# Kernel tuning notes

Hardware: AMD Instinct MI355X
Metric: run time of the kernel (lower is better)

Reference implementation:

```python
import jax, jax.numpy as jnp
import numpy as np

TOKEN_DIM = 256
NUM_HEADS = 2
IN_DIMS = 512
D = TOKEN_DIM * NUM_HEADS  # 512
SCALE = TOKEN_DIM ** (-0.5)


def _l2norm(v, axis):
    # torch F.normalize: v / max(||v||_2, eps)
    n = jnp.sqrt(jnp.sum(v * v, axis=axis, keepdims=True))
    return v / jnp.maximum(n, 1e-12)


def setup_inputs() -> dict:
    key = jax.random.key(0)
    ks = jax.random.split(key, 10)
    b, n = 8, 4096
    x = jax.random.normal(ks[0], (b, n, IN_DIMS), dtype=jnp.float32)
    s = 0.02
    Wq = jax.random.normal(ks[1], (IN_DIMS, D), dtype=jnp.float32) * s
    bq = jax.random.normal(ks[2], (D,), dtype=jnp.float32) * s
    Wk = jax.random.normal(ks[3], (IN_DIMS, D), dtype=jnp.float32) * s
    bk = jax.random.normal(ks[4], (D,), dtype=jnp.float32) * s
    Wr = jax.random.normal(ks[5], (D, TOKEN_DIM), dtype=jnp.float32) * s
    br = jax.random.normal(ks[6], (TOKEN_DIM,), dtype=jnp.float32) * s
    w_alpha = jax.random.normal(ks[7], (D, 1), dtype=jnp.float32)
    w_beta = jax.random.normal(ks[8], (D, 1), dtype=jnp.float32)
    return {"x": x, "Wq": Wq, "bq": bq, "Wk": Wk, "bk": bk,
            "Wr": Wr, "br": br, "w_alpha": w_alpha, "w_beta": w_beta}


def reference(x, Wq, bq, Wk, bk, Wr, br, w_alpha, w_beta):
    # x: [b, n, in_dims]
    q = x @ Wq + bq                      # [b, n, D]
    k = x @ Wk + bk                      # [b, n, D]
    q = _l2norm(q, axis=-1)
    k = _l2norm(k, axis=-1)
    v = _l2norm(k, axis=-1)              # original bug: value = normalize(key)

    alpha_w = (q @ w_alpha) * SCALE      # [b, n, 1]
    alpha_w = _l2norm(alpha_w, axis=1)   # normalize over token axis
    g_q = jnp.sum(alpha_w * q, axis=1)   # [b, D]
    g_q = jax.nn.softmax(g_q, axis=-1)

    p = g_q[:, None, :] * k              # [b, n, D]
    beta_w = _l2norm((p @ w_beta) * SCALE, axis=1)  # [b, n, 1]
    g_k = jnp.sum(beta_w * p, axis=1)    # [b, D]
    g_k = jax.nn.softmax(g_k, axis=-1)

    kvi = g_k[:, None, :] * v + q        # [b, n, D]
    return kvi @ Wr + br                 # [b, n, token_dim]
```

## Files before the change

kernel.cpp:

```cpp
#include <hip/hip_runtime.h>
#include <hip/hip_bf16.h>
#include <stdint.h>

#define BATCH    8
#define NTOKB    4096
#define NTOK     (BATCH * NTOKB)
#define DIN      512
#define DD       512
#define TD       256
#define SCALE    0.0625f
#define LSTR     36

typedef unsigned short ushortT;
typedef __attribute__((ext_vector_type(8))) short  short8;
typedef __attribute__((ext_vector_type(4))) float  f32x4;

union Frag { uint4 u; short8 s; };

__device__ __forceinline__ float bf_lo(uint32_t u) { return __uint_as_float(u << 16); }
__device__ __forceinline__ float bf_hi(uint32_t u) { return __uint_as_float(u & 0xffff0000u); }
__device__ __forceinline__ float bf2f(ushortT u) { return __uint_as_float(((uint32_t)u) << 16); }
__device__ __forceinline__ ushortT f2bf(float f) {
    uint32_t u = __float_as_uint(f);
    return (ushortT)((u + 0x7fffu + ((u >> 16) & 1u)) >> 16);
}
__device__ __forceinline__ short8 lds_frag(const ushortT* p) {
    uint2 a = *reinterpret_cast<const uint2*>(p);
    uint2 b = *reinterpret_cast<const uint2*>(p + 4);
    Frag f; f.u.x = a.x; f.u.y = a.y; f.u.z = b.x; f.u.w = b.y;
    return f.s;
}

__global__ __launch_bounds__(256) void packw_kernel(
    const float* __restrict__ Wq, const float* __restrict__ Wk,
    const float* __restrict__ Wr, ushortT* __restrict__ W16)
{
    const int blk = blockIdx.x;
    if (blk < 32) {
        const int mat = blk >> 4, c = blk & 15;
        const float* S = mat ? Wk : Wq;
        ushortT* D = W16 + (size_t)mat * (512 * 512) + (size_t)c * 16384;
        for (int i = threadIdx.x; i < 16384; i += 256) {
            int n = i & 511, kk = i >> 9;
            D[n * 32 + kk] = f2bf(S[(size_t)(c * 32 + kk) * 512 + n]);
        }
    } else {
        const int c = blk - 32;
        ushortT* D = W16 + (size_t)2 * (512 * 512) + (size_t)c * 8192;
        for (int i = threadIdx.x; i < 8192; i += 256) {
            int n = i & 255, kk = i >> 8;
            D[n * 32 + kk] = f2bf(Wr[(size_t)(c * 32 + kk) * 256 + n]);
        }
    }
}

__global__ __launch_bounds__(512) void gemm_qk_kernel(
    const float* __restrict__ x, const ushortT* __restrict__ W16,
    const float* __restrict__ bq, const float* __restrict__ bk,
    const float* __restrict__ w_alpha,
    ushortT* __restrict__ qn, ushortT* __restrict__ kn,
    float* __restrict__ alpha_raw)
{
    __shared__ ushortT xs[64 * LSTR];
    __shared__ ushortT wsd[512 * LSTR];
    __shared__ float rowsq[8][64];
    __shared__ float alphap[8][64];
    __shared__ float rnorm_s[64];

    const int tid = threadIdx.x;
    const int mat = blockIdx.y;
    const size_t tok0 = (size_t)blockIdx.x * 64;
    const ushortT* Wb = W16 + (size_t)mat * (512 * 512);
    const float* bias = mat ? bk : bq;
    ushortT* dst = mat ? kn : qn;

    const int lane = tid & 63, w = tid >> 6;
    const int m = lane & 15, quad = lane >> 4;

    f32x4 acc[4][4];
    #pragma unroll
    for (int tr = 0; tr < 4; ++tr)
        #pragma unroll
        for (int tc = 0; tc < 4; ++tc) acc[tr][tc] = (f32x4){0.f, 0.f, 0.f, 0.f};

    const int xtok = tid >> 3;
    const int xkg  = (tid & 7) * 4;
    const float* xsrc = x + (tok0 + xtok) * DIN;
    const int wr_r = tid >> 2;
    const int wseg = (tid & 3) * 8;

    for (int c = 0; c < 16; ++c) {
        __syncthreads();
        {
            float4 xv = *reinterpret_cast<const float4*>(xsrc + c * 32 + xkg);
            ushort4 xb;
            xb.x = f2bf(xv.x); xb.y = f2bf(xv.y); xb.z = f2bf(xv.z); xb.w = f2bf(xv.w);
            *reinterpret_cast<ushort4*>(&xs[xtok * LSTR + xkg]) = xb;
        }
        #pragma unroll
        for (int rr = 0; rr < 4; ++rr) {
            int r = wr_r + rr * 128;
            uint4 gv = *reinterpret_cast<const uint4*>(Wb + (size_t)c * 16384 + r * 32 + wseg);
            uint2* lp = reinterpret_cast<uint2*>(&wsd[r * LSTR + wseg]);
            lp[0] = make_uint2(gv.x, gv.y);
            lp[1] = make_uint2(gv.z, gv.w);
        }
        __syncthreads();
        {
            short8 af[4], bf[4];
            #pragma unroll
            for (int tr = 0; tr < 4; ++tr)
                af[tr] = lds_frag(&xs[(tr * 16 + m) * LSTR + quad * 8]);
            #pragma unroll
            for (int tc = 0; tc < 4; ++tc)
                bf[tc] = lds_frag(&wsd[(w * 64 + tc * 16 + m) * LSTR + quad * 8]);
            #pragma unroll
            for (int tr = 0; tr < 4; ++tr)
                #pragma unroll
                for (int tc = 0; tc < 4; ++tc)
                    acc[tr][tc] = __builtin_amdgcn_mfma_f32_16x16x32_bf16(af[tr], bf[tc], acc[tr][tc], 0, 0, 0);
        }
    }

    float biasv[4], wa[4];
    #pragma unroll
    for (int tc = 0; tc < 4; ++tc) {
        biasv[tc] = bias[w * 64 + tc * 16 + m];
        wa[tc] = (mat == 0) ? w_alpha[w * 64 + tc * 16 + m] : 0.f;
    }
    #pragma unroll
    for (int tr = 0; tr < 4; ++tr)
        #pragma unroll
        for (int tc = 0; tc < 4; ++tc)
            #pragma unroll
            for (int reg = 0; reg < 4; ++reg)
                acc[tr][tc][reg] += biasv[tc];

    __syncthreads();
    #pragma unroll
    for (int tr = 0; tr < 4; ++tr) {
        #pragma unroll
        for (int reg = 0; reg < 4; ++reg) {
            float s = 0.f, a = 0.f;
            #pragma unroll
            for (int tc = 0; tc < 4; ++tc) {
                float v = acc[tr][tc][reg];
                s = fmaf(v, v, s);
                a = fmaf(v, wa[tc], a);
            }
            #pragma unroll
            for (int off = 1; off < 16; off <<= 1) {
                s += __shfl_xor(s, off);
                a += __shfl_xor(a, off);
            }
            if (m == 0) {
                rowsq[w][tr * 16 + quad * 4 + reg] = s;
                alphap[w][tr * 16 + quad * 4 + reg] = a;
            }
        }
    }
    __syncthreads();
    if (tid < 64) {
        float ss = 0.f, aa = 0.f;
        #pragma unroll
        for (int w2 = 0; w2 < 8; ++w2) { ss += rowsq[w2][tid]; aa += alphap[w2][tid]; }
        float rn = 1.0f / fmaxf(sqrtf(ss), 1e-12f);
        rnorm_s[tid] = rn;
        if (mat == 0) alpha_raw[tok0 + tid] = SCALE * aa * rn;
    }
    __syncthreads();
    #pragma unroll
    for (int tr = 0; tr < 4; ++tr) {
        #pragma unroll
        for (int reg = 0; reg < 4; ++reg) {
            float rn = rnorm_s[tr * 16 + quad * 4 + reg];
            size_t row = tok0 + tr * 16 + quad * 4 + reg;
            ushortT* rp = dst + row * DD + w * 64 + m;
            #pragma unroll
            for (int tc = 0; tc < 4; ++tc)
                rp[tc * 16] = f2bf(acc[tr][tc][reg] * rn);
        }
    }
}

__global__ __launch_bounds__(256) void norm_kernel(const float* __restrict__ in,
                                                   float* __restrict__ inv_out)
{
    int b = blockIdx.x;
    __shared__ float red[256];
    float s = 0.f;
    for (int i = threadIdx.x; i < NTOKB; i += 256) {
        float v = in[b * NTOKB + i];
        s = fmaf(v, v, s);
    }
    red[threadIdx.x] = s;
    __syncthreads();
    for (int off = 128; off > 0; off >>= 1) {
        if (threadIdx.x < off) red[threadIdx.x] += red[threadIdx.x + off];
        __syncthreads();
    }
    if (threadIdx.x == 0) inv_out[b] = 1.0f / fmaxf(sqrtf(red[0]), 1e-12f);
}

__global__ __launch_bounds__(256) void wsum_kernel(const ushortT* __restrict__ M,
                                                   const float* __restrict__ raw,
                                                   const float* __restrict__ invp,
                                                   float* __restrict__ dst)
{
    const int blk = blockIdx.x, tid = threadIdx.x;
    const int b = blk >> 5;
    const int i0 = (blk & 31) * 128;
    __shared__ float wr[128];
    if (tid < 128) wr[tid] = raw[(size_t)b * NTOKB + i0 + tid];
    __syncthreads();
    const uint32_t* M32 = reinterpret_cast<const uint32_t*>(M);
    size_t base = ((size_t)b * NTOKB + i0) * 256 + tid;
    float a0 = 0.f, a1 = 0.f;
    for (int ii = 0; ii < 128; ++ii) {
        uint32_t v = M32[base + (size_t)ii * 256];
        float wv = wr[ii];
        a0 = fmaf(wv, bf_lo(v), a0);
        a1 = fmaf(wv, bf_hi(v), a1);
    }
    float iv = invp[b];
    atomicAdd(&dst[b * DD + 2 * tid],     a0 * iv);
    atomicAdd(&dst[b * DD + 2 * tid + 1], a1 * iv);
}

__global__ __launch_bounds__(256) void softmax_kernel(const float* __restrict__ in,
                                                      const float* __restrict__ mul,
                                                      const float* __restrict__ wbeta,
                                                      float* __restrict__ out,
                                                      float* __restrict__ wb2)
{
    int b = blockIdx.x, tid = threadIdx.x;
    __shared__ float red[256];
    float v0 = in[b * DD + tid], v1 = in[b * DD + 256 + tid];
    if (mul) { v0 *= mul[b * DD + tid]; v1 *= mul[b * DD + 256 + tid]; }
    red[tid] = fmaxf(v0, v1);
    __syncthreads();
    for (int off = 128; off > 0; off >>= 1) {
        if (tid < off) red[tid] = fmaxf(red[tid], red[tid + off]);
        __syncthreads();
    }
    float m = red[0];
    __syncthreads();
    float e0 = expf(v0 - m), e1 = expf(v1 - m);
    red[tid] = e0 + e1;
    __syncthreads();
    for (int off = 128; off > 0; off >>= 1) {
        if (tid < off) red[tid] += red[tid + off];
        __syncthreads();
    }
    float rs = 1.0f / red[0];
    float o0 = e0 * rs, o1 = e1 * rs;
    out[b * DD + tid] = o0;
    out[b * DD + 256 + tid] = o1;
    if (wb2) {
        wb2[b * DD + tid]       = o0 * wbeta[tid];
        wb2[b * DD + 256 + tid] = o1 * wbeta[256 + tid];
    }
}

__global__ __launch_bounds__(256) void beta_kernel(const ushortT* __restrict__ kn,
                                                   const float* __restrict__ wb2,
                                                   float* __restrict__ beta_raw)
{
    int wave = threadIdx.x >> 6, lane = threadIdx.x & 63;
    size_t tok = (size_t)blockIdx.x * 4 + wave;
    int b = (int)(tok >> 12);
    uint4 kv = *reinterpret_cast<const uint4*>(kn + tok * DD + lane * 8);
    float4 wv0 = *reinterpret_cast<const float4*>(wb2 + b * DD + lane * 8);
    float4 wv1 = *reinterpret_cast<const float4*>(wb2 + b * DD + lane * 8 + 4);
    float s = bf_lo(kv.x) * wv0.x + bf_hi(kv.x) * wv0.y
            + bf_lo(kv.y) * wv0.z + bf_hi(kv.y) * wv0.w
            + bf_lo(kv.z) * wv1.x + bf_hi(kv.z) * wv1.y
            + bf_lo(kv.w) * wv1.z + bf_hi(kv.w) * wv1.w;
    #pragma unroll
    for (int off = 32; off > 0; off >>= 1) s += __shfl_xor(s, off);
    if (lane == 0) beta_raw[tok] = SCALE * s;
}

__global__ __launch_bounds__(256) void out_mfma_kernel(
    const ushortT* __restrict__ qn, const ushortT* __restrict__ kn,
    const float* __restrict__ g_k, const ushortT* __restrict__ WrT,
    const float* __restrict__ br, float* __restrict__ out)
{
    __shared__ ushortT kvs[64 * LSTR];
    __shared__ ushortT wrs[256 * LSTR];
    __shared__ float gks[512];

    const int tid = threadIdx.x;
    const size_t tok0 = (size_t)blockIdx.x * 64;
    const int b = (int)(tok0 >> 12);

    gks[tid] = g_k[b * DD + tid];
    gks[256 + tid] = g_k[b * DD + 256 + tid];

    const int lane = tid & 63, w = tid >> 6;
    const int m = lane & 15, quad = lane >> 4;

    f32x4 acc[4][4];
    #pragma unroll
    for (int tr = 0; tr < 4; ++tr)
        #pragma unroll
        for (int tc = 0; tc < 4; ++tc) acc[tr][tc] = (f32x4){0.f, 0.f, 0.f, 0.f};

    const int st  = tid >> 2;
    const int skg = (tid & 3) * 8;
    const int wr_r = tid >> 2;
    const int wseg = (tid & 3) * 8;

    for (int c = 0; c < 16; ++c) {
        __syncthreads();
        {
            const size_t base = (tok0 + st) * DD + c * 32 + skg;
            uint4 qv = *reinterpret_cast<const uint4*>(qn + base);
            uint4 kv = *reinterpret_cast<const uint4*>(kn + base);
            const float* g = &gks[c * 32 + skg];
            ushortT o[8];
            o[0] = f2bf(fmaf(g[0], bf_lo(kv.x), bf_lo(qv.x)));
            o[1] = f2bf(fmaf(g[1], bf_hi(kv.x), bf_hi(qv.x)));
            o[2] = f2bf(fmaf(g[2], bf_lo(kv.y), bf_lo(qv.y)));
            o[3] = f2bf(fmaf(g[3], bf_hi(kv.y), bf_hi(qv.y)));
            o[4] = f2bf(fmaf(g[4], bf_lo(kv.z), bf_lo(qv.z)));
            o[5] = f2bf(fmaf(g[5], bf_hi(kv.z), bf_hi(qv.z)));
            o[6] = f2bf(fmaf(g[6], bf_lo(kv.w), bf_lo(qv.w)));
            o[7] = f2bf(fmaf(g[7], bf_hi(kv.w), bf_hi(qv.w)));
            uint2* lp = reinterpret_cast<uint2*>(&kvs[st * LSTR + skg]);
            lp[0] = make_uint2(((uint32_t)o[1] << 16) | o[0], ((uint32_t)o[3] << 16) | o[2]);
            lp[1] = make_uint2(((uint32_t)o[5] << 16) | o[4], ((uint32_t)o[7] << 16) | o[6]);
        }
        #pragma unroll
        for (int rr = 0; rr < 4; ++rr) {
            int r = wr_r + rr * 64;
            uint4 gv = *reinterpret_cast<const uint4*>(WrT + (size_t)c * 8192 + r * 32 + wseg);
            uint2* lp = reinterpret_cast<uint2*>(&wrs[r * LSTR + wseg]);
            lp[0] = make_uint2(gv.x, gv.y);
            lp[1] = make_uint2(gv.z, gv.w);
        }
        __syncthreads();
        {
            short8 af[4], bfr[4];
            #pragma unroll
            for (int tr = 0; tr < 4; ++tr)
                af[tr] = lds_frag(&kvs[(tr * 16 + m) * LSTR + quad * 8]);
            #pragma unroll
            for (int tc = 0; tc < 4; ++tc)
                bfr[tc] = lds_frag(&wrs[(w * 64 + tc * 16 + m) * LSTR + quad * 8]);
            #pragma unroll
            for (int tr = 0; tr < 4; ++tr)
                #pragma unroll
                for (int tc = 0; tc < 4; ++tc)
                    acc[tr][tc] = __builtin_amdgcn_mfma_f32_16x16x32_bf16(af[tr], bfr[tc], acc[tr][tc], 0, 0, 0);
        }
    }

    float brv[4];
    #pragma unroll
    for (int tc = 0; tc < 4; ++tc) brv[tc] = br[w * 64 + tc * 16 + m];
    #pragma unroll
    for (int tr = 0; tr < 4; ++tr) {
        #pragma unroll
        for (int reg = 0; reg < 4; ++reg) {
            size_t row = tok0 + tr * 16 + quad * 4 + reg;
            float* rp = out + row * TD + w * 64 + m;
            #pragma unroll
            for (int tc = 0; tc < 4; ++tc)
                rp[tc * 16] = acc[tr][tc][reg] + brv[tc];
        }
    }
}

extern "C" void kernel_launch(void* const* d_in, const int* in_sizes, int n_in,
                              void* d_out, int out_size, void* d_ws, size_t ws_size,
                              hipStream_t stream)
{
    const float* x       = (const float*)d_in[0];
    const float* Wq      = (const float*)d_in[1];
    const float* bq      = (const float*)d_in[2];
    const float* Wk      = (const float*)d_in[3];
    const float* bk      = (const float*)d_in[4];
    const float* Wr      = (const float*)d_in[5];
    const float* br      = (const float*)d_in[6];
    const float* w_alpha = (const float*)d_in[7];
    const float* w_beta  = (const float*)d_in[8];
    float* out = (float*)d_out;

    ushortT* kn = (ushortT*)d_out;

    char* ws = (char*)d_ws;
    ushortT* qn = (ushortT*)ws;        ws += (size_t)NTOK * DD * sizeof(ushortT);
    ushortT* W16 = (ushortT*)ws;       ws += (size_t)2 * 512 * 512 * sizeof(ushortT)
                                           + (size_t)512 * 256 * sizeof(ushortT);
    float* alpha_raw = (float*)ws;     ws += (size_t)NTOK * sizeof(float);
    float* beta_raw  = (float*)ws;     ws += (size_t)NTOK * sizeof(float);
    float* gq_raw = (float*)ws;        ws += (size_t)BATCH * DD * sizeof(float);
    float* h_raw  = (float*)ws;        ws += (size_t)BATCH * DD * sizeof(float);
    float* g_q    = (float*)ws;        ws += (size_t)BATCH * DD * sizeof(float);
    float* wb2    = (float*)ws;        ws += (size_t)BATCH * DD * sizeof(float);
    float* g_k    = (float*)ws;        ws += (size_t)BATCH * DD * sizeof(float);
    float* inv_a  = (float*)ws;        ws += 64;
    float* inv_b  = (float*)ws;        ws += 64;
    ushortT* WrT = W16 + (size_t)2 * 512 * 512;

    hipMemsetAsync(gq_raw, 0, 2 * BATCH * DD * sizeof(float), stream);

    packw_kernel<<<48, 256, 0, stream>>>(Wq, Wk, Wr, W16);
    gemm_qk_kernel<<<dim3(NTOK / 64, 2), 512, 0, stream>>>(x, W16, bq, bk, w_alpha, qn, kn, alpha_raw);
    norm_kernel<<<BATCH, 256, 0, stream>>>(alpha_raw, inv_a);
    wsum_kernel<<<256, 256, 0, stream>>>(qn, alpha_raw, inv_a, gq_raw);
    softmax_kernel<<<BATCH, 256, 0, stream>>>(gq_raw, nullptr, w_beta, g_q, wb2);
    beta_kernel<<<NTOK / 4, 256, 0, stream>>>(kn, wb2, beta_raw);
    norm_kernel<<<BATCH, 256, 0, stream>>>(beta_raw, inv_b);
    wsum_kernel<<<256, 256, 0, stream>>>(kn, beta_raw, inv_b, h_raw);
    softmax_kernel<<<BATCH, 256, 0, stream>>>(h_raw, g_q, nullptr, g_k, nullptr);
    out_mfma_kernel<<<NTOK / 64, 256, 0, stream>>>(qn, kn, g_k, WrT, br, out);
}
```

Before: 254.4 us.

## Load weight tiles directly into LDS with an XOR-swizzled layout

Weight tiles in both MFMA GEMM kernels are now copied with global_load_lds 16-byte direct-to-LDS loads, so they no longer pass through registers with separate LDS stores. The padded LDS stride is dropped. To avoid bank conflicts without padding, the packing kernel writes the weights pre-swizzled (XOR of the k-group with row bits), and the fragment reads undo the swizzle using single 16-byte LDS loads. This relies on the swizzle matching exactly between the pack and read sides, and on the direct-to-LDS builtin's per-wave addressing layout.

```diff
diff --git a/kernel.cpp b/kernel.cpp
--- a/kernel.cpp
+++ b/kernel.cpp
@@ -30,6 +30,12 @@
     Frag f; f.u.x = a.x; f.u.y = a.y; f.u.z = b.x; f.u.w = b.y;
     return f.s;
 }
+__device__ __forceinline__ void gload_lds16(const ushortT* g, ushortT* l) {
+    __builtin_amdgcn_global_load_lds(
+        (const __attribute__((address_space(1))) uint32_t*)(const void*)g,
+        (__attribute__((address_space(3))) uint32_t*)(void*)l,
+        16, 0, 0);
+}
 
 __global__ __launch_bounds__(256) void packw_kernel(
     const float* __restrict__ Wq, const float* __restrict__ Wk,
@@ -41,15 +47,17 @@
         const float* S = mat ? Wk : Wq;
         ushortT* D = W16 + (size_t)mat * (512 * 512) + (size_t)c * 16384;
         for (int i = threadIdx.x; i < 16384; i += 256) {
-            int n = i & 511, kk = i >> 9;
-            D[n * 32 + kk] = f2bf(S[(size_t)(c * 32 + kk) * 512 + n]);
+            int n = i & 511, p = i >> 9;
+            int l = ((p >> 3) ^ ((n >> 1) & 3)) * 8 + (p & 7);
+            D[n * 32 + p] = f2bf(S[(size_t)(c * 32 + l) * 512 + n]);
         }
     } else {
         const int c = blk - 32;
         ushortT* D = W16 + (size_t)2 * (512 * 512) + (size_t)c * 8192;
         for (int i = threadIdx.x; i < 8192; i += 256) {
-            int n = i & 255, kk = i >> 8;
-            D[n * 32 + kk] = f2bf(Wr[(size_t)(c * 32 + kk) * 256 + n]);
+            int n = i & 255, p = i >> 8;
+            int l = ((p >> 3) ^ ((n >> 1) & 3)) * 8 + (p & 7);
+            D[n * 32 + p] = f2bf(Wr[(size_t)(c * 32 + l) * 256 + n]);
         }
     }
 }
@@ -61,8 +69,8 @@
     ushortT* __restrict__ qn, ushortT* __restrict__ kn,
     float* __restrict__ alpha_raw)
 {
-    __shared__ ushortT xs[64 * LSTR];
-    __shared__ ushortT wsd[512 * LSTR];
+    __shared__ __align__(16) ushortT xs[64 * LSTR];
+    __shared__ __align__(16) ushortT wsd[512 * 32];
     __shared__ float rowsq[8][64];
     __shared__ float alphap[8][64];
     __shared__ float rnorm_s[64];
@@ -86,8 +94,6 @@
     const int xtok = tid >> 3;
     const int xkg  = (tid & 7) * 4;
     const float* xsrc = x + (tok0 + xtok) * DIN;
-    const int wr_r = tid >> 2;
-    const int wseg = (tid & 3) * 8;
 
     for (int c = 0; c < 16; ++c) {
         __syncthreads();
@@ -97,13 +103,13 @@
             xb.x = f2bf(xv.x); xb.y = f2bf(xv.y); xb.z = f2bf(xv.z); xb.w = f2bf(xv.w);
             *reinterpret_cast<ushort4*>(&xs[xtok * LSTR + xkg]) = xb;
         }
-        #pragma unroll
-        for (int rr = 0; rr < 4; ++rr) {
-            int r = wr_r + rr * 128;
-            uint4 gv = *reinterpret_cast<const uint4*>(Wb + (size_t)c * 16384 + r * 32 + wseg);
-            uint2* lp = reinterpret_cast<uint2*>(&wsd[r * LSTR + wseg]);
-            lp[0] = make_uint2(gv.x, gv.y);
-            lp[1] = make_uint2(gv.z, gv.w);
+        {
+            const ushortT* wsrc = Wb + (size_t)c * 16384;
+            #pragma unroll
+            for (int i = 0; i < 4; ++i) {
+                const int region = i * 8 + w;
+                gload_lds16(wsrc + region * 512 + lane * 8, &wsd[region * 512]);
+            }
         }
         __syncthreads();
         {
@@ -112,8 +118,11 @@
             for (int tr = 0; tr < 4; ++tr)
                 af[tr] = lds_frag(&xs[(tr * 16 + m) * LSTR + quad * 8]);
             #pragma unroll
-            for (int tc = 0; tc < 4; ++tc)
-                bf[tc] = lds_frag(&wsd[(w * 64 + tc * 16 + m) * LSTR + quad * 8]);
+            for (int tc = 0; tc < 4; ++tc) {
+                const int n = w * 64 + tc * 16 + m;
+                bf[tc] = *reinterpret_cast<const short8*>(
+                    &wsd[n * 32 + ((quad ^ ((n >> 1) & 3)) * 8)]);
+            }
             #pragma unroll
             for (int tr = 0; tr < 4; ++tr)
                 #pragma unroll
@@ -286,8 +295,8 @@
     const float* __restrict__ g_k, const ushortT* __restrict__ WrT,
     const float* __restrict__ br, float* __restrict__ out)
 {
-    __shared__ ushortT kvs[64 * LSTR];
-    __shared__ ushortT wrs[256 * LSTR];
+    __shared__ __align__(16) ushortT kvs[64 * LSTR];
+    __shared__ __align__(16) ushortT wrs[256 * 32];
     __shared__ float gks[512];
 
     const int tid = threadIdx.x;
@@ -308,8 +317,6 @@
 
     const int st  = tid >> 2;
     const int skg = (tid & 3) * 8;
-    const int wr_r = tid >> 2;
-    const int wseg = (tid & 3) * 8;
 
     for (int c = 0; c < 16; ++c) {
         __syncthreads();
@@ -331,13 +338,13 @@
             lp[0] = make_uint2(((uint32_t)o[1] << 16) | o[0], ((uint32_t)o[3] << 16) | o[2]);
             lp[1] = make_uint2(((uint32_t)o[5] << 16) | o[4], ((uint32_t)o[7] << 16) | o[6]);
         }
-        #pragma unroll
-        for (int rr = 0; rr < 4; ++rr) {
-            int r = wr_r + rr * 64;
-            uint4 gv = *reinterpret_cast<const uint4*>(WrT + (size_t)c * 8192 + r * 32 + wseg);
-            uint2* lp = reinterpret_cast<uint2*>(&wrs[r * LSTR + wseg]);
-            lp[0] = make_uint2(gv.x, gv.y);
-            lp[1] = make_uint2(gv.z, gv.w);
+        {
+            const ushortT* wsrc = WrT + (size_t)c * 8192;
+            #pragma unroll
+            for (int i = 0; i < 4; ++i) {
+                const int region = i * 4 + w;
+                gload_lds16(wsrc + region * 512 + lane * 8, &wrs[region * 512]);
+            }
         }
         __syncthreads();
         {
@@ -346,8 +353,11 @@
             for (int tr = 0; tr < 4; ++tr)
                 af[tr] = lds_frag(&kvs[(tr * 16 + m) * LSTR + quad * 8]);
             #pragma unroll
-            for (int tc = 0; tc < 4; ++tc)
-                bfr[tc] = lds_frag(&wrs[(w * 64 + tc * 16 + m) * LSTR + quad * 8]);
+            for (int tc = 0; tc < 4; ++tc) {
+                const int n = w * 64 + tc * 16 + m;
+                bfr[tc] = *reinterpret_cast<const short8*>(
+                    &wrs[n * 32 + ((quad ^ ((n >> 1) & 3)) * 8)]);
+            }
             #pragma unroll
             for (int tr = 0; tr < 4; ++tr)
                 #pragma unroll
```

Result: faster. 247.7 us (-2.6%).

## Stage full A tile in LDS once and stream weight fragments from global into registers

Applied to the files above, without the earlier changes.

Both MFMA GEMM kernels now load the whole 64xK activation tile into LDS up front with a padded stride, instead of staging per 32-wide K chunk. Weight B fragments are read straight from global memory into registers, double-buffered across K steps, so the weight LDS staging and the two per-chunk barriers go away. The aim is to cut synchronisation and LDS traffic and to overlap weight loads with MFMA work. In exchange, LDS use per block goes up (about 66KB), which may limit occupancy, and the weight reads now depend on L2/global latency being hidden.

```diff
diff --git a/kernel.cpp b/kernel.cpp
--- a/kernel.cpp
+++ b/kernel.cpp
@@ -9,26 +9,38 @@
 #define DD       512
 #define TD       256
 #define SCALE    0.0625f
-#define LSTR     36
+#define XP       520
 
 typedef unsigned short ushortT;
 typedef __attribute__((ext_vector_type(8))) short  short8;
 typedef __attribute__((ext_vector_type(4))) float  f32x4;
 
-union Frag { uint4 u; short8 s; };
-
 __device__ __forceinline__ float bf_lo(uint32_t u) { return __uint_as_float(u << 16); }
 __device__ __forceinline__ float bf_hi(uint32_t u) { return __uint_as_float(u & 0xffff0000u); }
-__device__ __forceinline__ float bf2f(ushortT u) { return __uint_as_float(((uint32_t)u) << 16); }
 __device__ __forceinline__ ushortT f2bf(float f) {
     uint32_t u = __float_as_uint(f);
     return (ushortT)((u + 0x7fffu + ((u >> 16) & 1u)) >> 16);
 }
-__device__ __forceinline__ short8 lds_frag(const ushortT* p) {
-    uint2 a = *reinterpret_cast<const uint2*>(p);
-    uint2 b = *reinterpret_cast<const uint2*>(p + 4);
-    Frag f; f.u.x = a.x; f.u.y = a.y; f.u.z = b.x; f.u.w = b.y;
-    return f.s;
+
+template<int CHSTR>
+__device__ __forceinline__ void k_step(
+    const ushortT* xbase, const ushortT* __restrict__ wbase,
+    int c, int pc, bool preload, short8* breg, f32x4 (&acc)[4][4])
+{
+    short8 af[4];
+    #pragma unroll
+    for (int tr = 0; tr < 4; ++tr)
+        af[tr] = *reinterpret_cast<const short8*>(xbase + tr * 16 * XP + c * 32);
+    #pragma unroll
+    for (int tc = 0; tc < 4; ++tc) {
+        #pragma unroll
+        for (int tr = 0; tr < 4; ++tr)
+            acc[tr][tc] = __builtin_amdgcn_mfma_f32_16x16x32_bf16(
+                af[tr], breg[tc], acc[tr][tc], 0, 0, 0);
+        if (preload)
+            breg[tc] = *reinterpret_cast<const short8*>(
+                wbase + (size_t)pc * CHSTR + tc * 512);
+    }
 }
 
 __global__ __launch_bounds__(256) void packw_kernel(
@@ -54,15 +66,14 @@
     }
 }
 
-__global__ __launch_bounds__(512) void gemm_qk_kernel(
+__global__ __launch_bounds__(512, 4) void gemm_qk_kernel(
     const float* __restrict__ x, const ushortT* __restrict__ W16,
     const float* __restrict__ bq, const float* __restrict__ bk,
     const float* __restrict__ w_alpha,
     ushortT* __restrict__ qn, ushortT* __restrict__ kn,
     float* __restrict__ alpha_raw)
 {
-    __shared__ ushortT xs[64 * LSTR];
-    __shared__ ushortT wsd[512 * LSTR];
+    __shared__ __align__(16) ushortT xs[64 * XP];
     __shared__ float rowsq[8][64];
     __shared__ float alphap[8][64];
     __shared__ float rnorm_s[64];
@@ -77,50 +88,43 @@
     const int lane = tid & 63, w = tid >> 6;
     const int m = lane & 15, quad = lane >> 4;
 
+    const ushortT* wbase = Wb + (w * 64 + m) * 32 + quad * 8;
+    short8 bA[4], bB[4];
+    #pragma unroll
+    for (int tc = 0; tc < 4; ++tc)
+        bA[tc] = *reinterpret_cast<const short8*>(wbase + tc * 512);
+    #pragma unroll
+    for (int tc = 0; tc < 4; ++tc)
+        bB[tc] = *reinterpret_cast<const short8*>(wbase + 16384 + tc * 512);
+
+    {
+        const int xtok = tid >> 3;
+        const int xk4  = (tid & 7) * 4;
+        const float* xsrc = x + (tok0 + xtok) * DIN;
+        #pragma unroll 4
+        for (int c = 0; c < 16; ++c) {
+            float4 v = *reinterpret_cast<const float4*>(xsrc + c * 32 + xk4);
+            ushort4 b4;
+            b4.x = f2bf(v.x); b4.y = f2bf(v.y); b4.z = f2bf(v.z); b4.w = f2bf(v.w);
+            *reinterpret_cast<ushort4*>(&xs[xtok * XP + c * 32 + xk4]) = b4;
+        }
+    }
+
     f32x4 acc[4][4];
     #pragma unroll
     for (int tr = 0; tr < 4; ++tr)
         #pragma unroll
         for (int tc = 0; tc < 4; ++tc) acc[tr][tc] = (f32x4){0.f, 0.f, 0.f, 0.f};
 
-    const int xtok = tid >> 3;
-    const int xkg  = (tid & 7) * 4;
-    const float* xsrc = x + (tok0 + xtok) * DIN;
-    const int wr_r = tid >> 2;
-    const int wseg = (tid & 3) * 8;
-
-    for (int c = 0; c < 16; ++c) {
-        __syncthreads();
-        {
-            float4 xv = *reinterpret_cast<const float4*>(xsrc + c * 32 + xkg);
-            ushort4 xb;
-            xb.x = f2bf(xv.x); xb.y = f2bf(xv.y); xb.z = f2bf(xv.z); xb.w = f2bf(xv.w);
-            *reinterpret_cast<ushort4*>(&xs[xtok * LSTR + xkg]) = xb;
-        }
-        #pragma unroll
-        for (int rr = 0; rr < 4; ++rr) {
-            int r = wr_r + rr * 128;
-            uint4 gv = *reinterpret_cast<const uint4*>(Wb + (size_t)c * 16384 + r * 32 + wseg);
-            uint2* lp = reinterpret_cast<uint2*>(&wsd[r * LSTR + wseg]);
-            lp[0] = make_uint2(gv.x, gv.y);
-            lp[1] = make_uint2(gv.z, gv.w);
-        }
-        __syncthreads();
-        {
-            short8 af[4], bf[4];
-            #pragma unroll
-            for (int tr = 0; tr < 4; ++tr)
-                af[tr] = lds_frag(&xs[(tr * 16 + m) * LSTR + quad * 8]);
-            #pragma unroll
-            for (int tc = 0; tc < 4; ++tc)
-                bf[tc] = lds_frag(&wsd[(w * 64 + tc * 16 + m) * LSTR + quad * 8]);
-            #pragma unroll
-            for (int tr = 0; tr < 4; ++tr)
-                #pragma unroll
-                for (int tc = 0; tc < 4; ++tc)
-                    acc[tr][tc] = __builtin_amdgcn_mfma_f32_16x16x32_bf16(af[tr], bf[tc], acc[tr][tc], 0, 0, 0);
-        }
-    }
+    __syncthreads();
+
+    const ushortT* xbase = xs + m * XP + quad * 8;
+    for (int cc = 0; cc < 14; cc += 2) {
+        k_step<16384>(xbase, wbase, cc,     cc + 2, true,  bA, acc);
+        k_step<16384>(xbase, wbase, cc + 1, cc + 3, true,  bB, acc);
+    }
+    k_step<16384>(xbase, wbase, 14, 0, false, bA, acc);
+    k_step<16384>(xbase, wbase, 15, 0, false, bB, acc);
 
     float biasv[4], wa[4];
     #pragma unroll
@@ -136,7 +140,6 @@
             for (int reg = 0; reg < 4; ++reg)
                 acc[tr][tc][reg] += biasv[tc];
 
-    __syncthreads();
     #pragma unroll
     for (int tr = 0; tr < 4; ++tr) {
         #pragma unroll
@@ -286,8 +289,7 @@
     const float* __restrict__ g_k, const ushortT* __restrict__ WrT,
     const float* __restrict__ br, float* __restrict__ out)
 {
-    __shared__ ushortT kvs[64 * LSTR];
-    __shared__ ushortT wrs[256 * LSTR];
+    __shared__ __align__(16) ushortT kvs[64 * XP];
     __shared__ float gks[512];
 
     const int tid = threadIdx.x;
@@ -300,61 +302,61 @@
     const int lane = tid & 63, w = tid >> 6;
     const int m = lane & 15, quad = lane >> 4;
 
-    f32x4 acc[4][4];
-    #pragma unroll
-    for (int tr = 0; tr < 4; ++tr)
-        #pragma unroll
-        for (int tc = 0; tc < 4; ++tc) acc[tr][tc] = (f32x4){0.f, 0.f, 0.f, 0.f};
+    const ushortT* wbase = WrT + (w * 64 + m) * 32 + quad * 8;
+    short8 bA[4], bB[4];
+    #pragma unroll
+    for (int tc = 0; tc < 4; ++tc)
+        bA[tc] = *reinterpret_cast<const short8*>(wbase + tc * 512);
+    #pragma unroll
+    for (int tc = 0; tc < 4; ++tc)
+        bB[tc] = *reinterpret_cast<const short8*>(wbase + 8192 + tc * 512);
 
     const int st  = tid >> 2;
     const int skg = (tid & 3) * 8;
-    const int wr_r = tid >> 2;
-    const int wseg = (tid & 3) * 8;
+    const ushortT* qrow = qn + (tok0 + st) * DD + skg;
+    const ushortT* krow = kn + (tok0 + st) * DD + skg;
+
+    uint4 qvA = *reinterpret_cast<const uint4*>(qrow);
+    uint4 kvA = *reinterpret_cast<const uint4*>(krow);
+    __syncthreads();
 
     for (int c = 0; c < 16; ++c) {
-        __syncthreads();
-        {
-            const size_t base = (tok0 + st) * DD + c * 32 + skg;
-            uint4 qv = *reinterpret_cast<const uint4*>(qn + base);
-            uint4 kv = *reinterpret_cast<const uint4*>(kn + base);
-            const float* g = &gks[c * 32 + skg];
-            ushortT o[8];
-            o[0] = f2bf(fmaf(g[0], bf_lo(kv.x), bf_lo(qv.x)));
-            o[1] = f2bf(fmaf(g[1], bf_hi(kv.x), bf_hi(qv.x)));
-            o[2] = f2bf(fmaf(g[2], bf_lo(kv.y), bf_lo(qv.y)));
-            o[3] = f2bf(fmaf(g[3], bf_hi(kv.y), bf_hi(qv.y)));
-            o[4] = f2bf(fmaf(g[4], bf_lo(kv.z), bf_lo(qv.z)));
-            o[5] = f2bf(fmaf(g[5], bf_hi(kv.z), bf_hi(qv.z)));
-            o[6] = f2bf(fmaf(g[6], bf_lo(kv.w), bf_lo(qv.w)));
-            o[7] = f2bf(fmaf(g[7], bf_hi(kv.w), bf_hi(qv.w)));
-            uint2* lp = reinterpret_cast<uint2*>(&kvs[st * LSTR + skg]);
-            lp[0] = make_uint2(((uint32_t)o[1] << 16) | o[0], ((uint32_t)o[3] << 16) | o[2]);
-            lp[1] = make_uint2(((uint32_t)o[5] << 16) | o[4], ((uint32_t)o[7] << 16) | o[6]);
-        }
-        #pragma unroll
-        for (int rr = 0; rr < 4; ++rr) {
-            int r = wr_r + rr * 64;
-            uint4 gv = *reinterpret_cast<const uint4*>(WrT + (size_t)c * 8192 + r * 32 + wseg);
-            uint2* lp = reinterpret_cast<uint2*>(&wrs[r * LSTR + wseg]);
-            lp[0] = make_uint2(gv.x, gv.y);
-            lp[1] = make_uint2(gv.z, gv.w);
-        }
-        __syncthreads();
-        {
-            short8 af[4], bfr[4];
-            #pragma unroll
-            for (int tr = 0; tr < 4; ++tr)
-                af[tr] = lds_frag(&kvs[(tr * 16 + m) * LSTR + quad * 8]);
-            #pragma unroll
-            for (int tc = 0; tc < 4; ++tc)
-                bfr[tc] = lds_frag(&wrs[(w * 64 + tc * 16 + m) * LSTR + quad * 8]);
-            #pragma unroll
-            for (int tr = 0; tr < 4; ++tr)
-                #pragma unroll
-                for (int tc = 0; tc < 4; ++tc)
-                    acc[tr][tc] = __builtin_amdgcn_mfma_f32_16x16x32_bf16(af[tr], bfr[tc], acc[tr][tc], 0, 0, 0);
-        }
-    }
+        uint4 qvB, kvB;
+        if (c + 1 < 16) {
+            qvB = *reinterpret_cast<const uint4*>(qrow + (c + 1) * 32);
+            kvB = *reinterpret_cast<const uint4*>(krow + (c + 1) * 32);
+        }
+        const float* g = &gks[c * 32 + skg];
+        ushortT o[8];
+        o[0] = f2bf(fmaf(g[0], bf_lo(kvA.x), bf_lo(qvA.x)));
+        o[1] = f2bf(fmaf(g[1], bf_hi(kvA.x), bf_hi(qvA.x)));
+        o[2] = f2bf(fmaf(g[2], bf_lo(kvA.y), bf_lo(qvA.y)));
+        o[3] = f2bf(fmaf(g[3], bf_hi(kvA.y), bf_hi(qvA.y)));
+        o[4] = f2bf(fmaf(g[4], bf_lo(kvA.z), bf_lo(qvA.z)));
+        o[5] = f2bf(fmaf(g[5], bf_hi(kvA.z), bf_hi(qvA.z)));
+        o[6] = f2bf(fmaf(g[6], bf_lo(kvA.w), bf_lo(qvA.w)));
+        o[7] = f2bf(fmaf(g[7], bf_hi(kvA.w), bf_hi(qvA.w)));
+        uint2* lp = reinterpret_cast<uint2*>(&kvs[st * XP + c * 32 + skg]);
+        lp[0] = make_uint2(((uint32_t)o[1] << 16) | o[0], ((uint32_t)o[3] << 16) | o[2]);
+        lp[1] = make_uint2(((uint32_t)o[5] << 16) | o[4], ((uint32_t)o[7] << 16) | o[6]);
+        qvA = qvB; kvA = kvB;
+    }
+
+    f32x4 acc[4][4];
+    #pragma unroll
+    for (int tr = 0; tr < 4; ++tr)
+        #pragma unroll
+        for (int tc = 0; tc < 4; ++tc) acc[tr][tc] = (f32x4){0.f, 0.f, 0.f, 0.f};
+
+    __syncthreads();
+
+    const ushortT* xbase = kvs + m * XP + quad * 8;
+    for (int cc = 0; cc < 14; cc += 2) {
+        k_step<8192>(xbase, wbase, cc,     cc + 2, true,  bA, acc);
+        k_step<8192>(xbase, wbase, cc + 1, cc + 3, true,  bB, acc);
+    }
+    k_step<8192>(xbase, wbase, 14, 0, false, bA, acc);
+    k_step<8192>(xbase, wbase, 15, 0, false, bB, acc);
 
     float brv[4];
     #pragma unroll
```

New measurement: 256.0 us. Within noise of the previous version (+0.6%).
